# Performance work log

Hardware: AMD Instinct MI355X
Metric: run time of the kernel (lower is better)

The kernel has to match this reference:

```python
import jax, jax.numpy as jnp
import numpy as np

N_NODES = 100000
N_EDGES = 800000
IN_DIM, HID_DIM, OUT_DIM = 128, 256, 128


def setup_inputs() -> dict:
    key = jax.random.key(0)
    k1, k2, k3, k4, k5 = jax.random.split(key, 5)
    x = jax.random.normal(k1, (N_NODES, IN_DIM), dtype=jnp.float32)
    edge_index = jax.random.randint(k2, (2, N_EDGES), 0, N_NODES, dtype=jnp.int64)
    edge_weight = jax.random.uniform(k3, (N_EDGES,), dtype=jnp.float32)
    W1 = jax.random.normal(k4, (IN_DIM, HID_DIM), dtype=jnp.float32) * 0.02
    b1 = jnp.zeros((HID_DIM,), dtype=jnp.float32)
    W2 = jax.random.normal(k5, (HID_DIM, OUT_DIM), dtype=jnp.float32) * 0.02
    b2 = jnp.zeros((OUT_DIM,), dtype=jnp.float32)
    return {"x": x, "edge_index": edge_index, "edge_weight": edge_weight,
            "W1": W1, "b1": b1, "W2": W2, "b2": b2}


def reference(x, edge_index, edge_weight, W1, b1, W2, b2):
    # GCNConv (normalize=True, add_self_loops=False), two layers with ReLU.
    # Dropout is identity at inference.
    row = edge_index[0]  # source nodes (E,)
    col = edge_index[1]  # target nodes (E,)
    n = x.shape[0]

    # Symmetric normalization: deg at target, norm = d^-1/2[row]*w*d^-1/2[col]
    deg = jax.ops.segment_sum(edge_weight, col, num_segments=n)  # (N,)
    dis = jnp.where(deg > 0, jax.lax.rsqrt(deg), 0.0)
    norm = dis[row] * edge_weight * dis[col]  # (E,)

    def gcn_conv(h, W, b):
        h = h @ W                                   # (N, F_out)
        msg = h[row] * norm[:, None]                # (E, F_out) gather+scale
        agg = jax.ops.segment_sum(msg, col, num_segments=n)  # scatter-add
        return agg + b

    h = jax.nn.relu(gcn_conv(x.astype(jnp.float32), W1, b1))
    return gcn_conv(h, W2, b2)
```

## Files before the change

### kernel.cpp

```cpp
#include <hip/hip_runtime.h>
#include <hip/hip_bf16.h>
#include <cstdint>
#include <cstddef>

#define N_NODES 100000
#define N_EDGES 800000
#define IN_DIM 128
#define HID_DIM 256
#define OUT_DIM 128

typedef __attribute__((ext_vector_type(8))) short bf16x8;
typedef __attribute__((ext_vector_type(4))) float f32x4;

__device__ __forceinline__ unsigned short f32_to_bf16(float f) {
    __hip_bfloat16 b = __float2bfloat16(f);
    return *reinterpret_cast<unsigned short*>(&b);
}
__device__ __forceinline__ float bf16_lo(uint32_t u) {
    uint32_t v = u << 16; return *reinterpret_cast<float*>(&v);
}
__device__ __forceinline__ float bf16_hi(uint32_t u) {
    uint32_t v = u & 0xffff0000u; return *reinterpret_cast<float*>(&v);
}

__global__ void rank_hist_kernel(const int* __restrict__ ei,
                                 int* __restrict__ cnt,
                                 int* __restrict__ rank) {
    int e = blockIdx.x * 256 + threadIdx.x;
    if (e >= N_EDGES) return;
    rank[e] = atomicAdd(&cnt[ei[N_EDGES + e]], 1);
}

__global__ void scan1_kernel(const int* __restrict__ in, int* __restrict__ out,
                             int* __restrict__ bsums, int n) {
    __shared__ int tmp[256];
    int t = threadIdx.x;
    int i = blockIdx.x * 256 + t;
    int v = (i < n) ? in[i] : 0;
    tmp[t] = v;
    __syncthreads();
    for (int off = 1; off < 256; off <<= 1) {
        int u = (t >= off) ? tmp[t - off] : 0;
        __syncthreads();
        tmp[t] += u;
        __syncthreads();
    }
    if (i < n) out[i] = tmp[t] - v;
    if (t == 255) bsums[blockIdx.x] = tmp[255];
}

__global__ void scan2_kernel(int* __restrict__ bsums, int nb) {
    __shared__ int tmp[512];
    int t = threadIdx.x;
    int v = (t < nb) ? bsums[t] : 0;
    tmp[t] = v;
    __syncthreads();
    for (int off = 1; off < 512; off <<= 1) {
        int u = (t >= off) ? tmp[t - off] : 0;
        __syncthreads();
        tmp[t] += u;
        __syncthreads();
    }
    if (t < nb) bsums[t] = tmp[t] - v;
}

__global__ void scan3_kernel(int* __restrict__ rowp, const int* __restrict__ bsums,
                             int n, int total) {
    int i = blockIdx.x * 256 + threadIdx.x;
    if (i == 0) rowp[n] = total;
    if (i >= n) return;
    rowp[i] += bsums[blockIdx.x];
}

__global__ void place_kernel(const int* __restrict__ ei,
                             const float* __restrict__ ew,
                             const int* __restrict__ rank,
                             const int* __restrict__ rowp,
                             int2* __restrict__ pairs) {
    int e = blockIdx.x * 256 + threadIdx.x;
    if (e >= N_EDGES) return;
    int c = ei[N_EDGES + e];
    int pos = rowp[c] + rank[e];
    pairs[pos] = make_int2(ei[e], __float_as_int(ew[e]));
}

__global__ void deg_dis_kernel(const int* __restrict__ rowp,
                               const int2* __restrict__ pairs,
                               float* __restrict__ dis) {
    int v = blockIdx.x * 256 + threadIdx.x;
    if (v >= N_NODES) return;
    int b = rowp[v], e = rowp[v + 1];
    float d = 0.f;
    for (int j = b; j < e; ++j) d += __int_as_float(pairs[j].y);
    dis[v] = d > 0.f ? rsqrtf(d) : 0.f;
}

__global__ void prep_kernel(const float* __restrict__ x, uint32_t* __restrict__ xb,
                            const float* __restrict__ W1, unsigned short* __restrict__ W1T,
                            const float* __restrict__ W2, unsigned short* __restrict__ W2T) {
    int b = blockIdx.x;
    if (b < 12500) {
        int i = b * 256 + threadIdx.x;
        float4 v = ((const float4*)x)[i];
        uint32_t lo = (uint32_t)f32_to_bf16(v.x) | ((uint32_t)f32_to_bf16(v.y) << 16);
        uint32_t hi = (uint32_t)f32_to_bf16(v.z) | ((uint32_t)f32_to_bf16(v.w) << 16);
        ((uint2*)xb)[i] = make_uint2(lo, hi);
    } else if (b < 12628) {
        int idx = (b - 12500) * 256 + threadIdx.x;
        int r = idx >> 8, c = idx & 255;
        W1T[c * IN_DIM + r] = f32_to_bf16(W1[idx]);
    } else {
        int idx = (b - 12628) * 256 + threadIdx.x;
        int r = idx >> 7, c = idx & 127;
        W2T[c * HID_DIM + r] = f32_to_bf16(W2[idx]);
    }
}

template <bool OUT_BF16>
__global__ void aggregate_kernel(const uint2* __restrict__ feat,
                                 const int* __restrict__ rowp,
                                 const int2* __restrict__ pairs,
                                 const float* __restrict__ dis,
                                 void* __restrict__ out_v,
                                 const float* __restrict__ bias) {
    int gtid = blockIdx.x * blockDim.x + threadIdx.x;
    int node = gtid >> 5;
    int lane = threadIdx.x & 31;
    if (node >= N_NODES) return;
    int beg = rowp[node], end = rowp[node + 1];
    float dv = dis[node];
    float ax = 0.f, ay = 0.f, az = 0.f, aw = 0.f;

    int j = beg;
    for (; j + 4 <= end; j += 4) {
        int2 p[4]; uint2 u[4]; float d[4];
        #pragma unroll
        for (int q = 0; q < 4; ++q) p[q] = pairs[j + q];
        #pragma unroll
        for (int q = 0; q < 4; ++q) {
            u[q] = feat[(size_t)p[q].x * 32 + lane];
            d[q] = dis[p[q].x];
        }
        #pragma unroll
        for (int q = 0; q < 4; ++q) {
            float w = __int_as_float(p[q].y) * d[q] * dv;
            ax += w * bf16_lo(u[q].x); ay += w * bf16_hi(u[q].x);
            az += w * bf16_lo(u[q].y); aw += w * bf16_hi(u[q].y);
        }
    }
    if (j + 2 <= end) {
        int2 p0 = pairs[j], p1 = pairs[j + 1];
        uint2 u0 = feat[(size_t)p0.x * 32 + lane];
        uint2 u1 = feat[(size_t)p1.x * 32 + lane];
        float w0 = __int_as_float(p0.y) * dis[p0.x] * dv;
        float w1 = __int_as_float(p1.y) * dis[p1.x] * dv;
        ax += w0 * bf16_lo(u0.x) + w1 * bf16_lo(u1.x);
        ay += w0 * bf16_hi(u0.x) + w1 * bf16_hi(u1.x);
        az += w0 * bf16_lo(u0.y) + w1 * bf16_lo(u1.y);
        aw += w0 * bf16_hi(u0.y) + w1 * bf16_hi(u1.y);
        j += 2;
    }
    if (j < end) {
        int2 p0 = pairs[j];
        uint2 u0 = feat[(size_t)p0.x * 32 + lane];
        float w0 = __int_as_float(p0.y) * dis[p0.x] * dv;
        ax += w0 * bf16_lo(u0.x); ay += w0 * bf16_hi(u0.x);
        az += w0 * bf16_lo(u0.y); aw += w0 * bf16_hi(u0.y);
    }
    if (bias) {
        float4 b = ((const float4*)bias)[lane];
        ax += b.x; ay += b.y; az += b.z; aw += b.w;
    }
    if (OUT_BF16) {
        uint2 o;
        o.x = (uint32_t)f32_to_bf16(ax) | ((uint32_t)f32_to_bf16(ay) << 16);
        o.y = (uint32_t)f32_to_bf16(az) | ((uint32_t)f32_to_bf16(aw) << 16);
        ((uint2*)out_v)[(size_t)node * 32 + lane] = o;
    } else {
        ((float4*)out_v)[(size_t)node * 32 + lane] = make_float4(ax, ay, az, aw);
    }
}

__global__ __launch_bounds__(256) void gemm_fused_kernel(
    const unsigned short* __restrict__ A,
    const unsigned short* __restrict__ W1T,
    const float* __restrict__ b1,
    const unsigned short* __restrict__ W2T,
    unsigned short* __restrict__ T,
    int M) {
    __shared__ unsigned short As[128 * 128];
    __shared__ unsigned short Hs[128 * 136];
    int tid = threadIdx.x;
    int wave = tid >> 6, lane = tid & 63;
    int m0 = blockIdx.x * 128;
    int wr = (wave & 1) * 64, wc = (wave >> 1) * 64;
    int fr = lane & 15, fq = lane >> 4;

    #pragma unroll
    for (int i = 0; i < 8; ++i) {
        int cbase = (i * 4 + wave) * 64;
        int c = cbase + lane;
        int m = c >> 4, cl = c & 15;
        int qg = ((cl & 7) ^ (m & 7)) | (cl & 8);
        int gm = m0 + m; if (gm >= M) gm = M - 1;
        const unsigned short* ga = A + (size_t)gm * 128 + qg * 8;
        __builtin_amdgcn_global_load_lds(
            (const __attribute__((address_space(1))) void*)ga,
            (__attribute__((address_space(3))) void*)(As + (size_t)cbase * 8),
            16, 0, 0);
    }
    __syncthreads();

    f32x4 acc_t[4][4] = {};
    #pragma unroll
    for (int nh = 0; nh < 2; ++nh) {
        f32x4 acc_h[4][4] = {};
        #pragma unroll
        for (int ks = 0; ks < 4; ++ks) {
            int q = ks * 4 + fq;
            int cl = ((q & 7) ^ (fr & 7)) | (q & 8);
            bf16x8 af[4], wf[4];
            #pragma unroll
            for (int mt = 0; mt < 4; ++mt)
                af[mt] = *(const bf16x8*)(As + (wr + mt * 16 + fr) * 128 + cl * 8);
            #pragma unroll
            for (int nt = 0; nt < 4; ++nt)
                wf[nt] = *(const bf16x8*)(W1T +
                    (size_t)(nh * 128 + wc + nt * 16 + fr) * 128 + ks * 32 + fq * 8);
            #pragma unroll
            for (int mt = 0; mt < 4; ++mt)
                #pragma unroll
                for (int nt = 0; nt < 4; ++nt)
                    acc_h[mt][nt] = __builtin_amdgcn_mfma_f32_16x16x32_bf16(
                        af[mt], wf[nt], acc_h[mt][nt], 0, 0, 0);
        }
        float bv[4];
        #pragma unroll
        for (int nt = 0; nt < 4; ++nt) bv[nt] = b1[nh * 128 + wc + nt * 16 + fr];
        __syncthreads();
        #pragma unroll
        for (int mt = 0; mt < 4; ++mt)
            #pragma unroll
            for (int r = 0; r < 4; ++r) {
                int row = wr + mt * 16 + fq * 4 + r;
                #pragma unroll
                for (int nt = 0; nt < 4; ++nt) {
                    float v = fmaxf(acc_h[mt][nt][r] + bv[nt], 0.f);
                    Hs[row * 136 + wc + nt * 16 + fr] = f32_to_bf16(v);
                }
            }
        __syncthreads();
        #pragma unroll
        for (int ks = 0; ks < 4; ++ks) {
            bf16x8 hf[4], wf[4];
            #pragma unroll
            for (int mt = 0; mt < 4; ++mt)
                hf[mt] = *(const bf16x8*)(Hs + (wr + mt * 16 + fr) * 136 + ks * 32 + fq * 8);
            #pragma unroll
            for (int nt = 0; nt < 4; ++nt)
                wf[nt] = *(const bf16x8*)(W2T +
                    (size_t)(wc + nt * 16 + fr) * 256 + nh * 128 + ks * 32 + fq * 8);
            #pragma unroll
            for (int mt = 0; mt < 4; ++mt)
                #pragma unroll
                for (int nt = 0; nt < 4; ++nt)
                    acc_t[mt][nt] = __builtin_amdgcn_mfma_f32_16x16x32_bf16(
                        hf[mt], wf[nt], acc_t[mt][nt], 0, 0, 0);
        }
    }

    #pragma unroll
    for (int mt = 0; mt < 4; ++mt)
        #pragma unroll
        for (int r = 0; r < 4; ++r) {
            int row = m0 + wr + mt * 16 + fq * 4 + r;
            if (row >= M) continue;
            #pragma unroll
            for (int nt = 0; nt < 4; ++nt)
                T[(size_t)row * 128 + wc + nt * 16 + fr] = f32_to_bf16(acc_t[mt][nt][r]);
        }
}

extern "C" void kernel_launch(void* const* d_in, const int* in_sizes, int n_in,
                              void* d_out, int out_size, void* d_ws, size_t ws_size,
                              hipStream_t stream) {
    const float* x  = (const float*)d_in[0];
    const int*   ei = (const int*)d_in[1];
    const float* ew = (const float*)d_in[2];
    const float* W1 = (const float*)d_in[3];
    const float* b1 = (const float*)d_in[4];
    const float* W2 = (const float*)d_in[5];
    const float* b2 = (const float*)d_in[6];
    float* out = (float*)d_out;

    char* ws = (char*)d_ws;
    size_t off = 0;
    auto alloc = [&](size_t bytes) -> void* {
        void* p = ws + off;
        off = (off + bytes + 255) & ~(size_t)255;
        return p;
    };
    int*   cnt   = (int*)  alloc((size_t)N_NODES * 4);
    float* dis   = (float*)alloc((size_t)N_NODES * 4);
    int*   rowp  = (int*)  alloc((size_t)(N_NODES + 1) * 4);
    int*   bsums = (int*)  alloc(512 * 4);
    int*   rank  = (int*)  alloc((size_t)N_EDGES * 4);
    int2*  pairs = (int2*) alloc((size_t)N_EDGES * 8);
    uint32_t* xb = (uint32_t*)alloc((size_t)N_NODES * IN_DIM * 2);
    unsigned short* W1T = (unsigned short*)alloc((size_t)IN_DIM * HID_DIM * 2);
    unsigned short* W2T = (unsigned short*)alloc((size_t)HID_DIM * OUT_DIM * 2);
    unsigned short* A1  = (unsigned short*)alloc((size_t)N_NODES * IN_DIM * 2);
    unsigned short* t   = (unsigned short*)alloc((size_t)N_NODES * OUT_DIM * 2);

    hipMemsetAsync(cnt, 0, (size_t)N_NODES * 4, stream);

    int ne_blocks = (N_EDGES + 255) / 256;
    int nn_blocks = (N_NODES + 255) / 256;

    rank_hist_kernel<<<ne_blocks, 256, 0, stream>>>(ei, cnt, rank);
    scan1_kernel<<<nn_blocks, 256, 0, stream>>>(cnt, rowp, bsums, N_NODES);
    scan2_kernel<<<1, 512, 0, stream>>>(bsums, nn_blocks);
    scan3_kernel<<<nn_blocks, 256, 0, stream>>>(rowp, bsums, N_NODES, N_EDGES);
    place_kernel<<<ne_blocks, 256, 0, stream>>>(ei, ew, rank, rowp, pairs);
    deg_dis_kernel<<<nn_blocks, 256, 0, stream>>>(rowp, pairs, dis);
    prep_kernel<<<12756, 256, 0, stream>>>(x, xb, W1, W1T, W2, W2T);

    int agg_blocks = (N_NODES * 32) / 256;

    aggregate_kernel<true><<<agg_blocks, 256, 0, stream>>>(
        (const uint2*)xb, rowp, pairs, dis, A1, nullptr);

    gemm_fused_kernel<<<(N_NODES + 127) / 128, 256, 0, stream>>>(
        A1, W1T, b1, W2T, t, N_NODES);

    aggregate_kernel<false><<<agg_blocks, 256, 0, stream>>>(
        (const uint2*)t, rowp, pairs, dis, out, b2);
}
```

Measured before the change: 297.9 us.

## Pre-swizzle weights into MFMA fragment order and hoist A fragments

The prep kernel now writes W1 and W2 in bf16 in the exact per-lane MFMA fragment order. The fused GEMM can then load weight fragments as fully coalesced 16-byte vectors indexed by lane, instead of strided row reads. The A-tile fragments are read from LDS once into registers before the loop over the two hidden halves, so they are not reloaded for each half. Launch bounds are raised to request two blocks per CU, which limits register use while more fragments are now kept live, so spilling is a risk.

```diff
diff --git a/kernel.cpp b/kernel.cpp
--- a/kernel.cpp
+++ b/kernel.cpp
@@ -96,8 +96,8 @@
 }
 
 __global__ void prep_kernel(const float* __restrict__ x, uint32_t* __restrict__ xb,
-                            const float* __restrict__ W1, unsigned short* __restrict__ W1T,
-                            const float* __restrict__ W2, unsigned short* __restrict__ W2T) {
+                            const float* __restrict__ W1, unsigned short* __restrict__ W1F,
+                            const float* __restrict__ W2, unsigned short* __restrict__ W2F) {
     int b = blockIdx.x;
     if (b < 12500) {
         int i = b * 256 + threadIdx.x;
@@ -107,12 +107,22 @@
         ((uint2*)xb)[i] = make_uint2(lo, hi);
     } else if (b < 12628) {
         int idx = (b - 12500) * 256 + threadIdx.x;
-        int r = idx >> 8, c = idx & 255;
-        W1T[c * IN_DIM + r] = f32_to_bf16(W1[idx]);
+        int j = idx & 7, lane = (idx >> 3) & 63;
+        int nt = (idx >> 9) & 3, ks = (idx >> 11) & 3;
+        int wc = (idx >> 13) & 1, nh = (idx >> 14) & 1;
+        int fr = lane & 15, fq = lane >> 4;
+        int row = nh * 128 + wc * 64 + nt * 16 + fr;
+        int kk = ks * 32 + fq * 8 + j;
+        W1F[idx] = f32_to_bf16(W1[kk * HID_DIM + row]);
     } else {
         int idx = (b - 12628) * 256 + threadIdx.x;
-        int r = idx >> 7, c = idx & 127;
-        W2T[c * HID_DIM + r] = f32_to_bf16(W2[idx]);
+        int j = idx & 7, lane = (idx >> 3) & 63;
+        int nt = (idx >> 9) & 3, ks = (idx >> 11) & 3;
+        int wc = (idx >> 13) & 1, nh = (idx >> 14) & 1;
+        int fr = lane & 15, fq = lane >> 4;
+        int n = wc * 64 + nt * 16 + fr;
+        int kk = nh * 128 + ks * 32 + fq * 8 + j;
+        W2F[idx] = f32_to_bf16(W2[kk * OUT_DIM + n]);
     }
 }
 
@@ -181,11 +191,11 @@
     }
 }
 
-__global__ __launch_bounds__(256) void gemm_fused_kernel(
+__global__ __launch_bounds__(256, 2) void gemm_fused_kernel(
     const unsigned short* __restrict__ A,
-    const unsigned short* __restrict__ W1T,
+    const unsigned short* __restrict__ W1F,
     const float* __restrict__ b1,
-    const unsigned short* __restrict__ W2T,
+    const unsigned short* __restrict__ W2F,
     unsigned short* __restrict__ T,
     int M) {
     __shared__ unsigned short As[128 * 128];
@@ -193,7 +203,9 @@
     int tid = threadIdx.x;
     int wave = tid >> 6, lane = tid & 63;
     int m0 = blockIdx.x * 128;
-    int wr = (wave & 1) * 64, wc = (wave >> 1) * 64;
+    int wr = (wave & 1) * 64;
+    int wcid = wave >> 1;
+    int wc = wcid * 64;
     int fr = lane & 15, fq = lane >> 4;
 
     #pragma unroll
@@ -211,28 +223,36 @@
     }
     __syncthreads();
 
+    bf16x8 af[4][4];
+    #pragma unroll
+    for (int ks = 0; ks < 4; ++ks) {
+        int q = ks * 4 + fq;
+        int cl = ((q & 7) ^ (fr & 7)) | (q & 8);
+        #pragma unroll
+        for (int mt = 0; mt < 4; ++mt)
+            af[ks][mt] = *(const bf16x8*)(As + (wr + mt * 16 + fr) * 128 + cl * 8);
+    }
+
+    const bf16x8* w1p = (const bf16x8*)W1F;
+    const bf16x8* w2p = (const bf16x8*)W2F;
+
     f32x4 acc_t[4][4] = {};
     #pragma unroll
     for (int nh = 0; nh < 2; ++nh) {
+        int wbase = (nh * 2 + wcid) * 16 * 64;
         f32x4 acc_h[4][4] = {};
         #pragma unroll
         for (int ks = 0; ks < 4; ++ks) {
-            int q = ks * 4 + fq;
-            int cl = ((q & 7) ^ (fr & 7)) | (q & 8);
-            bf16x8 af[4], wf[4];
-            #pragma unroll
-            for (int mt = 0; mt < 4; ++mt)
-                af[mt] = *(const bf16x8*)(As + (wr + mt * 16 + fr) * 128 + cl * 8);
+            bf16x8 wf[4];
             #pragma unroll
             for (int nt = 0; nt < 4; ++nt)
-                wf[nt] = *(const bf16x8*)(W1T +
-                    (size_t)(nh * 128 + wc + nt * 16 + fr) * 128 + ks * 32 + fq * 8);
+                wf[nt] = w1p[wbase + (ks * 4 + nt) * 64 + lane];
             #pragma unroll
             for (int mt = 0; mt < 4; ++mt)
                 #pragma unroll
                 for (int nt = 0; nt < 4; ++nt)
                     acc_h[mt][nt] = __builtin_amdgcn_mfma_f32_16x16x32_bf16(
-                        af[mt], wf[nt], acc_h[mt][nt], 0, 0, 0);
+                        af[ks][mt], wf[nt], acc_h[mt][nt], 0, 0, 0);
         }
         float bv[4];
         #pragma unroll
@@ -252,14 +272,13 @@
         __syncthreads();
         #pragma unroll
         for (int ks = 0; ks < 4; ++ks) {
-            bf16x8 hf[4], wf[4];
+            bf16x8 wf[4], hf[4];
+            #pragma unroll
+            for (int nt = 0; nt < 4; ++nt)
+                wf[nt] = w2p[wbase + (ks * 4 + nt) * 64 + lane];
             #pragma unroll
             for (int mt = 0; mt < 4; ++mt)
                 hf[mt] = *(const bf16x8*)(Hs + (wr + mt * 16 + fr) * 136 + ks * 32 + fq * 8);
-            #pragma unroll
-            for (int nt = 0; nt < 4; ++nt)
-                wf[nt] = *(const bf16x8*)(W2T +
-                    (size_t)(wc + nt * 16 + fr) * 256 + nh * 128 + ks * 32 + fq * 8);
             #pragma unroll
             for (int mt = 0; mt < 4; ++mt)
                 #pragma unroll
@@ -307,8 +326,8 @@
     int*   rank  = (int*)  alloc((size_t)N_EDGES * 4);
     int2*  pairs = (int2*) alloc((size_t)N_EDGES * 8);
     uint32_t* xb = (uint32_t*)alloc((size_t)N_NODES * IN_DIM * 2);
-    unsigned short* W1T = (unsigned short*)alloc((size_t)IN_DIM * HID_DIM * 2);
-    unsigned short* W2T = (unsigned short*)alloc((size_t)HID_DIM * OUT_DIM * 2);
+    unsigned short* W1F = (unsigned short*)alloc((size_t)IN_DIM * HID_DIM * 2);
+    unsigned short* W2F = (unsigned short*)alloc((size_t)HID_DIM * OUT_DIM * 2);
     unsigned short* A1  = (unsigned short*)alloc((size_t)N_NODES * IN_DIM * 2);
     unsigned short* t   = (unsigned short*)alloc((size_t)N_NODES * OUT_DIM * 2);
 
@@ -323,7 +342,7 @@
     scan3_kernel<<<nn_blocks, 256, 0, stream>>>(rowp, bsums, N_NODES, N_EDGES);
     place_kernel<<<ne_blocks, 256, 0, stream>>>(ei, ew, rank, rowp, pairs);
     deg_dis_kernel<<<nn_blocks, 256, 0, stream>>>(rowp, pairs, dis);
-    prep_kernel<<<12756, 256, 0, stream>>>(x, xb, W1, W1T, W2, W2T);
+    prep_kernel<<<12756, 256, 0, stream>>>(x, xb, W1, W1F, W2, W2F);
 
     int agg_blocks = (N_NODES * 32) / 256;
 
@@ -331,7 +350,7 @@
         (const uint2*)xb, rowp, pairs, dis, A1, nullptr);
 
     gemm_fused_kernel<<<(N_NODES + 127) / 128, 256, 0, stream>>>(
-        A1, W1T, b1, W2T, t, N_NODES);
+        A1, W1F, b1, W2F, t, N_NODES);
 
     aggregate_kernel<false><<<agg_blocks, 256, 0, stream>>>(
         (const uint2*)t, rowp, pairs, dis, out, b2);
```

Result: faster. 279.3 us (-6.2%).
